# Kernel tuning notes

Measured on AMD Instinct MI355X. Metric: run time of the kernel, lower is better.

Reference implementation:

```python
import jax, jax.numpy as jnp
import numpy as np

BSZ = 2048
L = 64            # sequence length, power of 2
D = 15            # symbol_repr_size
NC = 10           # n_classes; embedding row NC is the 'inf' token
TREE_LEN = 2 * L - 1  # next_power_of_2(L)*2 - 1


def rms_norm(x):
    # x / (sqrt(mean(x^2, -1) + 1e-6) + 1e-6)
    return x / (jnp.sqrt(jnp.mean(x * x, axis=-1, keepdims=True) + 1e-6) + 1e-6)


def setup_inputs() -> dict:
    key = jax.random.key(0)
    k1, k2, k3, k4, k5 = jax.random.split(key, 5)
    x = jax.random.randint(k1, (BSZ, L), 0, NC)
    q = jnp.sort(jax.random.randint(k2, (BSZ, 2), 0, L), axis=1)  # low <= high
    query_low, query_high = q[:, 0], q[:, 1]
    emb = jax.random.normal(k3, (NC + 1, D), dtype=jnp.float32)
    W_lin = jax.random.normal(k4, (NC, D), dtype=jnp.float32) * 0.26   # ~1/sqrt(D)
    W_rule = jax.random.normal(k5, (2, D * D), dtype=jnp.float32) * 0.066  # ~1/D
    return {"emb": emb, "W_lin": W_lin, "W_rule": W_rule,
            "x": x, "query_low": query_low, "query_high": query_high}


def reference(emb, W_lin, W_rule, x, query_low, query_high):
    def combine(a, b):
        # outer product [b, D, D] -> rule linear (225 -> 2) -> softmax mix
        inp = jnp.einsum('bi,bj->bij', a, b).reshape(a.shape[0], -1)
        alpha = jax.nn.softmax(inp @ W_rule.T, axis=-1)  # [b, 2]
        return alpha[:, :1] * a + alpha[:, 1:] * b

    def build(trees, lst, low, high, pos):
        # recursive segment-tree build; low/high/pos are static Python ints
        if low == high:
            return rms_norm(trees.at[:, pos, :].set(lst[:, low, :]))
        mid = (low + high) // 2
        trees = build(trees, lst, low, mid, 2 * pos + 1)
        trees = build(trees, lst, mid + 1, high, 2 * pos + 2)
        mix = combine(trees[:, 2 * pos + 1], trees[:, 2 * pos + 2])
        return rms_norm(trees.at[:, pos, :].set(mix))

    inf_raw = emb[NC]  # raw inf token used inside query (no rms_norm in torch)

    def query(trees, returns, low, high, pos):
        if pos >= TREE_LEN:
            return returns
        f = returns.dtype
        mA = ((query_low <= low) & (query_high >= high)).astype(f)[:, None]
        returns = mA * trees[:, pos] + (1 - mA) * returns
        mB = ((query_low > high) | (query_high < low)).astype(f)[:, None]
        returns = mB * inf_raw[None, :] + (1 - mB) * returns
        mC = (1 - mA) * (1 - mB)
        mid = (low + high) // 2
        a1 = query(trees, returns, low, mid, 2 * pos + 1)
        a2 = query(trees, returns, mid + 1, high, 2 * pos + 2)
        new = combine(a1, a2)
        return rms_norm(mC * new + (1 - mC) * returns)

    h = rms_norm(emb[x])                              # [BSZ, L, D]
    inf_n = rms_norm(emb[NC][None, None, :])          # normalized inf token
    trees = jnp.broadcast_to(inf_n, (BSZ, TREE_LEN, D)) + jnp.zeros((), emb.dtype)
    trees = build(trees, h, 0, L - 1, 0)              # [BSZ, TREE_LEN, D]
    returns = jnp.zeros((BSZ, D), dtype=emb.dtype)
    returns = query(trees, returns, 0, L - 1, 0)      # [BSZ, D]
    return returns @ W_lin.T                          # [BSZ, NC]
```

## Files before the change

### kernel.cpp

```cpp
#include <hip/hip_runtime.h>
#include <math.h>

#define DD 15
#define DP 20
#define LL 64
#define NCC 10
#define TL 127

__device__ __forceinline__ float dpp_xor1(float x) {
    return __int_as_float(__builtin_amdgcn_update_dpp(0, __float_as_int(x), 0xB1, 0xF, 0xF, true));
}
__device__ __forceinline__ float dpp_xor2(float x) {
    return __int_as_float(__builtin_amdgcn_update_dpp(0, __float_as_int(x), 0x4E, 0xF, 0xF, true));
}
__device__ __forceinline__ float dpp_hmirror(float x) {
    return __int_as_float(__builtin_amdgcn_update_dpp(0, __float_as_int(x), 0x141, 0xF, 0xF, true));
}

__device__ __forceinline__ void combine8_core(const float* Lrow, const float* Rrow,
                                              const float w[4][DD], int k, int qr, int u,
                                              float& o0, float& o1)
{
    float4 R0 = ((const float4*)Rrow)[0];
    float4 R1 = ((const float4*)Rrow)[1];
    float4 R2 = ((const float4*)Rrow)[2];
    float4 R3 = ((const float4*)Rrow)[3];
    float4 Aq = ((const float4*)Lrow)[qr];
    float Bv[DD] = {R0.x,R0.y,R0.z,R0.w, R1.x,R1.y,R1.z,R1.w,
                    R2.x,R2.y,R2.z,R2.w, R3.x,R3.y,R3.z};
    float Av[4] = {Aq.x, Aq.y, Aq.z, Aq.w};

    float p = 0.f;
    #pragma unroll
    for (int ri = 0; ri < 4; ++ri) {
        float d0 = 0.f;
        #pragma unroll
        for (int j = 0; j < DD; ++j) d0 = fmaf(w[ri][j], Bv[j], d0);
        p = fmaf(Av[ri], d0, p);
    }
    float a   = p + dpp_xor2(p);
    float hma = dpp_hmirror(a);
    float self = a + dpp_xor1(hma);
    float oth  = dpp_xor1(a) + hma;
    float mx = fmaxf(self, oth);
    float es = __expf(self - mx), eo = __expf(oth - mx);
    float rs = __builtin_amdgcn_rcpf(es + eo);
    float aS = es * rs, aO = eo * rs;
    float a0 = (k == 0) ? aS : aO;
    float a1 = (k == 0) ? aO : aS;

    float2 lm = ((const float2*)Lrow)[u];
    float2 rm = ((const float2*)Rrow)[u];
    float v0 = a0 * lm.x + a1 * rm.x;
    float v1 = a0 * lm.y + a1 * rm.y;
    float ss = v0 * v0 + v1 * v1;
    ss += dpp_xor1(ss);
    ss += dpp_xor2(ss);
    ss += dpp_hmirror(ss);
    float inv = __builtin_amdgcn_rsqf(ss * (1.0f / DD) + 1e-6f);
    o0 = v0 * inv; o1 = v1 * inv;
}

template<int LVL>
__device__ __forceinline__ void build_level(float (*tree)[DP], const float w[4][DD],
                                            int k, int qr, int u, int g)
{
    constexpr int n = 1 << LVL, first = n - 1, nst = (n + 7) / 8;
    #pragma unroll
    for (int st = 0; st < nst; ++st) {
        int pi0 = st * 8 + g;
        int pi = (n < 8) ? ((pi0 < n) ? pi0 : 0) : pi0;
        int p = first + pi;
        float o0, o1;
        combine8_core(&tree[2 * p + 1][0], &tree[2 * p + 2][0], w, k, qr, u, o0, o1);
        if (pi0 < n)
            ((float2*)&tree[p][0])[u] = make_float2(o0, o1);
    }
}

template<int LVL>
__device__ __forceinline__ void query_level(float (*tree)[DP], const float (*nemb)[DP],
                                            const float w[4][DD], int t, int k, int qr, int u,
                                            int ql, int qh)
{
    constexpr int first = (1 << LVL) - 1;
    constexpr int sh = 6 - LVL;
    constexpr int shc = sh - 1;
    const int g2 = (t >> 3) & 1;
    int bnd = g2 ? qh : ql;
    int pi = bnd >> sh;
    int lo = pi << sh, hi = lo + (1 << sh) - 1;
    bool full = (ql <= lo) && (qh >= hi);
    int p = first + pi;
    int ci1 = 2 * pi, ci2 = 2 * pi + 1;
    int lo1 = ci1 << shc, hi1 = lo1 + (1 << shc) - 1;
    int lo2 = ci2 << shc, hi2 = lo2 + (1 << shc) - 1;
    bool d1 = (ql > hi1) || (qh < lo1);
    bool d2 = (ql > hi2) || (qh < lo2);
    const float* Lrow = d1 ? &nemb[NCC][0] : &tree[2 * p + 1][0];
    const float* Rrow = d2 ? &nemb[NCC][0] : &tree[2 * p + 2][0];
    float o0, o1;
    combine8_core(Lrow, Rrow, w, k, qr, u, o0, o1);
    int pi_g0 = ql >> sh;
    bool we = (!full) && (t < 16) && (g2 == 0 || pi != pi_g0);
    if (we)
        ((float2*)&tree[p][0])[u] = make_float2(o0, o1);
}

extern "C" __global__ __attribute__((amdgpu_flat_work_group_size(64, 64)))
void seg_tree_kernel(
    const float* __restrict__ emb,
    const float* __restrict__ W_lin,
    const float* __restrict__ W_rule,
    const int*  __restrict__ x,
    const int*  __restrict__ qlo_g,
    const int*  __restrict__ qhi_g,
    float* __restrict__ out)
{
    __shared__ __align__(16) float nemb[NCC + 1][DP];
    __shared__ __align__(16) float tree[TL][DP];

    const int t = threadIdx.x;
    const int b = blockIdx.x;
    const int k = t & 1, qr = (t >> 1) & 3, u = t & 7, g = t >> 3;

    const int xi = x[b * LL + t];
    const int ql = qlo_g[b], qh = qhi_g[b];

    float w[4][DD];
    #pragma unroll
    for (int ri = 0; ri < 4; ++ri) {
        int i = 4 * qr + ri;
        bool valid = (i < DD);
        const float* src = W_rule + k * DD * DD + (valid ? i * DD : 0);
        #pragma unroll
        for (int j = 0; j < DD; ++j) w[ri][j] = valid ? src[j] : 0.0f;
    }
    #pragma unroll
    for (int ri = 0; ri < 4; ++ri)
        #pragma unroll
        for (int j = 0; j < DD; ++j)
            asm volatile("" : "+v"(w[ri][j]));

    float wl[DD];
    {
        const float* wlp = W_lin + ((t < NCC) ? t : 0) * DD;
        #pragma unroll
        for (int d = 0; d < DD; ++d) wl[d] = wlp[d];
        #pragma unroll
        for (int d = 0; d < DD; ++d) asm volatile("" : "+v"(wl[d]));
    }

    if (t < NCC + 1) {
        float v[DD]; float ssum = 0.f;
        #pragma unroll
        for (int d = 0; d < DD; ++d) { v[d] = emb[t * DD + d]; ssum += v[d] * v[d]; }
        float inv = __builtin_amdgcn_rsqf(ssum * (1.0f / DD) + 1e-6f);
        #pragma unroll
        for (int d = 0; d < DD; ++d) nemb[t][d] = v[d] * inv;
        nemb[t][DD] = 0.0f;
    }
    __syncthreads();

    #pragma unroll
    for (int j = 0; j < 4; ++j)
        ((float4*)&tree[63 + t][0])[j] = ((const float4*)&nemb[xi][0])[j];
    __syncthreads();

    build_level<5>(tree, w, k, qr, u, g);
    __syncthreads();
    build_level<4>(tree, w, k, qr, u, g);
    query_level<5>(tree, nemb, w, t, k, qr, u, ql, qh);
    __syncthreads();
    build_level<3>(tree, w, k, qr, u, g);
    query_level<4>(tree, nemb, w, t, k, qr, u, ql, qh);
    __syncthreads();
    build_level<2>(tree, w, k, qr, u, g);
    query_level<3>(tree, nemb, w, t, k, qr, u, ql, qh);
    __syncthreads();
    build_level<1>(tree, w, k, qr, u, g);
    query_level<2>(tree, nemb, w, t, k, qr, u, ql, qh);
    __syncthreads();
    build_level<0>(tree, w, k, qr, u, g);
    query_level<1>(tree, nemb, w, t, k, qr, u, ql, qh);
    __syncthreads();
    query_level<0>(tree, nemb, w, t, k, qr, u, ql, qh);
    __syncthreads();

    if (t < NCC) {
        float acc = 0.f;
        #pragma unroll
        for (int d = 0; d < DD; ++d) acc = fmaf(tree[0][d], wl[d], acc);
        out[b * NCC + t] = acc;
    }
}

extern "C" void kernel_launch(void* const* d_in, const int* in_sizes, int n_in,
                              void* d_out, int out_size, void* d_ws, size_t ws_size,
                              hipStream_t stream) {
    const float* emb    = (const float*)d_in[0];
    const float* W_lin  = (const float*)d_in[1];
    const float* W_rule = (const float*)d_in[2];
    const int*   x      = (const int*)d_in[3];
    const int*   qlo    = (const int*)d_in[4];
    const int*   qhi    = (const int*)d_in[5];
    float* outp = (float*)d_out;

    int bsz = in_sizes[3] / LL;
    seg_tree_kernel<<<dim3(bsz), dim3(64), 0, stream>>>(
        emb, W_lin, W_rule, x, qlo, qhi, outp);
}
```

Before: 16.33 us.

## Pack four batch elements per block, one wave each, and drop inter-level barriers

Each 256-thread block now processes four batch elements, one 64-lane wave per element, with a per-wave tree in LDS. All __syncthreads between tree levels are removed, relying on single-wave execution for ordering. The leaf level is no longer copied into shared memory: level-5 build and query read the normalized embeddings directly using per-thread token indices. The root build is dropped in favour of a specialized root query, and W_lin is read from global memory at the end instead of being held in registers. The aim is to cut barrier and launch overhead and LDS traffic. In exchange, correctness depends on intra-wave LDS ordering without explicit fences, and more threads now share each block's LDS.

```diff
diff --git a/kernel.cpp b/kernel.cpp
--- a/kernel.cpp
+++ b/kernel.cpp
@@ -5,7 +5,8 @@
 #define DP 20
 #define LL 64
 #define NCC 10
-#define TL 127
+#define NTREE 63
+#define EPB 4
 
 __device__ __forceinline__ float dpp_xor1(float x) {
     return __int_as_float(__builtin_amdgcn_update_dpp(0, __float_as_int(x), 0xB1, 0xF, 0xF, true));
@@ -38,8 +39,8 @@
         for (int j = 0; j < DD; ++j) d0 = fmaf(w[ri][j], Bv[j], d0);
         p = fmaf(Av[ri], d0, p);
     }
-    float a   = p + dpp_xor2(p);
-    float hma = dpp_hmirror(a);
+    float a    = p + dpp_xor2(p);
+    float hma  = dpp_hmirror(a);
     float self = a + dpp_xor1(hma);
     float oth  = dpp_xor1(a) + hma;
     float mx = fmaxf(self, oth);
@@ -61,8 +62,41 @@
     o0 = v0 * inv; o1 = v1 * inv;
 }
 
+__device__ __forceinline__ void build_level5(float (*tw)[DP], const float (*nemb)[DP],
+                                             const float w[4][DD],
+                                             const int xA[4], const int xB[4],
+                                             int k, int qr, int u, int g)
+{
+    #pragma unroll
+    for (int st = 0; st < 4; ++st) {
+        int pi = st * 8 + g;
+        float o0, o1;
+        combine8_core(&nemb[xA[st]][0], &nemb[xB[st]][0], w, k, qr, u, o0, o1);
+        ((float2*)&tw[31 + pi][0])[u] = make_float2(o0, o1);
+    }
+}
+
+__device__ __forceinline__ void query_level5(float (*tw)[DP], const float (*nemb)[DP],
+                                             const float w[4][DD], int t, int k, int qr, int u,
+                                             int ql, int qh, int xq1, int xq2)
+{
+    const int g2 = (t >> 3) & 1;
+    int bnd = g2 ? qh : ql;
+    int piB = bnd >> 1;
+    int lo = 2 * piB, hi = lo + 1;
+    bool full = (ql <= lo) && (qh >= hi);
+    bool d1 = (ql > lo) || (qh < lo);
+    bool d2 = (ql > hi) || (qh < hi);
+    const float* Lrow = d1 ? &nemb[NCC][0] : &nemb[xq1][0];
+    const float* Rrow = d2 ? &nemb[NCC][0] : &nemb[xq2][0];
+    float o0, o1;
+    combine8_core(Lrow, Rrow, w, k, qr, u, o0, o1);
+    bool we = (!full) && (t < 16) && (g2 == 0 || piB != (ql >> 1));
+    if (we) ((float2*)&tw[31 + piB][0])[u] = make_float2(o0, o1);
+}
+
 template<int LVL>
-__device__ __forceinline__ void build_level(float (*tree)[DP], const float w[4][DD],
+__device__ __forceinline__ void build_level(float (*tw)[DP], const float w[4][DD],
                                             int k, int qr, int u, int g)
 {
     constexpr int n = 1 << LVL, first = n - 1, nst = (n + 7) / 8;
@@ -72,14 +106,14 @@
         int pi = (n < 8) ? ((pi0 < n) ? pi0 : 0) : pi0;
         int p = first + pi;
         float o0, o1;
-        combine8_core(&tree[2 * p + 1][0], &tree[2 * p + 2][0], w, k, qr, u, o0, o1);
+        combine8_core(&tw[2 * p + 1][0], &tw[2 * p + 2][0], w, k, qr, u, o0, o1);
         if (pi0 < n)
-            ((float2*)&tree[p][0])[u] = make_float2(o0, o1);
+            ((float2*)&tw[p][0])[u] = make_float2(o0, o1);
     }
 }
 
 template<int LVL>
-__device__ __forceinline__ void query_level(float (*tree)[DP], const float (*nemb)[DP],
+__device__ __forceinline__ void query_level(float (*tw)[DP], const float (*nemb)[DP],
                                             const float w[4][DD], int t, int k, int qr, int u,
                                             int ql, int qh)
 {
@@ -97,17 +131,28 @@
     int lo2 = ci2 << shc, hi2 = lo2 + (1 << shc) - 1;
     bool d1 = (ql > hi1) || (qh < lo1);
     bool d2 = (ql > hi2) || (qh < lo2);
-    const float* Lrow = d1 ? &nemb[NCC][0] : &tree[2 * p + 1][0];
-    const float* Rrow = d2 ? &nemb[NCC][0] : &tree[2 * p + 2][0];
+    const float* Lrow = d1 ? &nemb[NCC][0] : &tw[2 * p + 1][0];
+    const float* Rrow = d2 ? &nemb[NCC][0] : &tw[2 * p + 2][0];
     float o0, o1;
     combine8_core(Lrow, Rrow, w, k, qr, u, o0, o1);
-    int pi_g0 = ql >> sh;
-    bool we = (!full) && (t < 16) && (g2 == 0 || pi != pi_g0);
-    if (we)
-        ((float2*)&tree[p][0])[u] = make_float2(o0, o1);
-}
-
-extern "C" __global__ __attribute__((amdgpu_flat_work_group_size(64, 64)))
+    bool we = (!full) && (t < 16) && (g2 == 0 || pi != (ql >> sh));
+    if (we) ((float2*)&tw[p][0])[u] = make_float2(o0, o1);
+}
+
+__device__ __forceinline__ void query_level0(float (*tw)[DP], const float (*nemb)[DP],
+                                             const float w[4][DD], int t, int k, int qr, int u,
+                                             int ql, int qh)
+{
+    bool d1 = (ql > 31);
+    bool d2 = (qh < 32);
+    const float* Lrow = d1 ? &nemb[NCC][0] : &tw[1][0];
+    const float* Rrow = d2 ? &nemb[NCC][0] : &tw[2][0];
+    float o0, o1;
+    combine8_core(Lrow, Rrow, w, k, qr, u, o0, o1);
+    if (t < 8) ((float2*)&tw[0][0])[u] = make_float2(o0, o1);
+}
+
+extern "C" __global__ __attribute__((amdgpu_flat_work_group_size(256, 256)))
 void seg_tree_kernel(
     const float* __restrict__ emb,
     const float* __restrict__ W_lin,
@@ -115,17 +160,31 @@
     const int*  __restrict__ x,
     const int*  __restrict__ qlo_g,
     const int*  __restrict__ qhi_g,
-    float* __restrict__ out)
+    float* __restrict__ out,
+    int bsz)
 {
     __shared__ __align__(16) float nemb[NCC + 1][DP];
-    __shared__ __align__(16) float tree[TL][DP];
-
-    const int t = threadIdx.x;
-    const int b = blockIdx.x;
+    __shared__ __align__(16) float tree[EPB][NTREE][DP];
+
+    const int tb = threadIdx.x;
+    const int wv = tb >> 6;
+    const int t  = tb & 63;
+    int b = blockIdx.x * EPB + wv;
+    const bool active = (b < bsz);
+    if (!active) b = bsz - 1;
+
     const int k = t & 1, qr = (t >> 1) & 3, u = t & 7, g = t >> 3;
-
-    const int xi = x[b * LL + t];
+    float (*tw)[DP] = tree[wv];
+
     const int ql = qlo_g[b], qh = qhi_g[b];
+    int xA[4], xB[4];
+    #pragma unroll
+    for (int st = 0; st < 4; ++st) {
+        xA[st] = x[b * LL + st * 16 + 2 * g];
+        xB[st] = x[b * LL + st * 16 + 2 * g + 1];
+    }
+    int piB = (((t >> 3) & 1) ? qh : ql) >> 1;
+    int xq1 = x[b * LL + 2 * piB], xq2 = x[b * LL + 2 * piB + 1];
 
     float w[4][DD];
     #pragma unroll
@@ -140,57 +199,40 @@
     for (int ri = 0; ri < 4; ++ri)
         #pragma unroll
         for (int j = 0; j < DD; ++j)
-            asm volatile("" : "+v"(w[ri][j]));
-
-    float wl[DD];
-    {
-        const float* wlp = W_lin + ((t < NCC) ? t : 0) * DD;
-        #pragma unroll
-        for (int d = 0; d < DD; ++d) wl[d] = wlp[d];
-        #pragma unroll
-        for (int d = 0; d < DD; ++d) asm volatile("" : "+v"(wl[d]));
-    }
-
-    if (t < NCC + 1) {
+            asm("" : "+v"(w[ri][j]));
+
+    if (tb < NCC + 1) {
         float v[DD]; float ssum = 0.f;
         #pragma unroll
-        for (int d = 0; d < DD; ++d) { v[d] = emb[t * DD + d]; ssum += v[d] * v[d]; }
+        for (int d = 0; d < DD; ++d) { v[d] = emb[tb * DD + d]; ssum += v[d] * v[d]; }
         float inv = __builtin_amdgcn_rsqf(ssum * (1.0f / DD) + 1e-6f);
         #pragma unroll
-        for (int d = 0; d < DD; ++d) nemb[t][d] = v[d] * inv;
-        nemb[t][DD] = 0.0f;
+        for (int d = 0; d < DD; ++d) nemb[tb][d] = v[d] * inv;
+        nemb[tb][DD] = 0.0f;
     }
     __syncthreads();
 
-    #pragma unroll
-    for (int j = 0; j < 4; ++j)
-        ((float4*)&tree[63 + t][0])[j] = ((const float4*)&nemb[xi][0])[j];
-    __syncthreads();
-
-    build_level<5>(tree, w, k, qr, u, g);
-    __syncthreads();
-    build_level<4>(tree, w, k, qr, u, g);
-    query_level<5>(tree, nemb, w, t, k, qr, u, ql, qh);
-    __syncthreads();
-    build_level<3>(tree, w, k, qr, u, g);
-    query_level<4>(tree, nemb, w, t, k, qr, u, ql, qh);
-    __syncthreads();
-    build_level<2>(tree, w, k, qr, u, g);
-    query_level<3>(tree, nemb, w, t, k, qr, u, ql, qh);
-    __syncthreads();
-    build_level<1>(tree, w, k, qr, u, g);
-    query_level<2>(tree, nemb, w, t, k, qr, u, ql, qh);
-    __syncthreads();
-    build_level<0>(tree, w, k, qr, u, g);
-    query_level<1>(tree, nemb, w, t, k, qr, u, ql, qh);
-    __syncthreads();
-    query_level<0>(tree, nemb, w, t, k, qr, u, ql, qh);
-    __syncthreads();
-
-    if (t < NCC) {
+    build_level5(tw, nemb, w, xA, xB, k, qr, u, g);
+    query_level5(tw, nemb, w, t, k, qr, u, ql, qh, xq1, xq2);
+
+    build_level<4>(tw, w, k, qr, u, g);
+    query_level<4>(tw, nemb, w, t, k, qr, u, ql, qh);
+
+    build_level<3>(tw, w, k, qr, u, g);
+    query_level<3>(tw, nemb, w, t, k, qr, u, ql, qh);
+
+    build_level<2>(tw, w, k, qr, u, g);
+    query_level<2>(tw, nemb, w, t, k, qr, u, ql, qh);
+
+    build_level<1>(tw, w, k, qr, u, g);
+    query_level<1>(tw, nemb, w, t, k, qr, u, ql, qh);
+
+    query_level0(tw, nemb, w, t, k, qr, u, ql, qh);
+
+    if (active && t < NCC) {
         float acc = 0.f;
         #pragma unroll
-        for (int d = 0; d < DD; ++d) acc = fmaf(tree[0][d], wl[d], acc);
+        for (int d = 0; d < DD; ++d) acc = fmaf(tw[0][d], W_lin[t * DD + d], acc);
         out[b * NCC + t] = acc;
     }
 }
@@ -207,6 +249,7 @@
     float* outp = (float*)d_out;
 
     int bsz = in_sizes[3] / LL;
-    seg_tree_kernel<<<dim3(bsz), dim3(64), 0, stream>>>(
-        emb, W_lin, W_rule, x, qlo, qhi, outp);
-}
+    int nblk = (bsz + EPB - 1) / EPB;
+    seg_tree_kernel<<<dim3(nblk), dim3(256), 0, stream>>>(
+        emb, W_lin, W_rule, x, qlo, qhi, outp, bsz);
+}
```

Result: faster. 15.33 us (-6.1%).
